# Optimization experiments

Measured on AMD Instinct MI355X. Metric: run time of the kernel, lower is better.

## Reference

```python
import jax, jax.numpy as jnp
import numpy as np

B, F, R, O = 32768, 64, 64, 64  # batch, in_features, rules, out_features


def setup_inputs() -> dict:
    key = jax.random.key(0)
    k1, k2, k3, k4, k5 = jax.random.split(key, 5)
    X = jax.random.normal(k1, (B, F), dtype=jnp.float32)
    tt = jax.random.normal(k2, (1, F, R), dtype=jnp.float32) * 0.01
    mean = jax.random.normal(k3, (1, F, R), dtype=jnp.float32)
    # std is a learned positive scale (set by _rule_initialization); keep it away from 0
    std = jax.random.uniform(k4, (1, F, R), dtype=jnp.float32, minval=0.5, maxval=1.5)
    W = jax.random.normal(k5, (O, R * (F + 1)), dtype=jnp.float32) * 0.02  # nn.Linear weight [out, in]
    return {"X": X, "tt": tt, "mean": mean, "std": std, "W": W}


def reference(X, tt, mean, std, W):
    t = jnp.tanh(tt)                                  # [1,F,R]
    z = (X[:, :, None] - mean) / std                  # [B,F,R]
    g = jnp.exp(-(z * z))                             # Gaussian membership [B,F,R]
    m = g * t + 0.5 * (1.0 - t)                       # affine blend toward 0.5
    fire = jnp.prod(m, axis=1)                        # product t-norm over features -> [B,R]
    w = fire / jnp.sum(fire, axis=1, keepdims=True)   # normalize over rules
    ones = jnp.ones((X.shape[0], 1), dtype=X.dtype)
    Xa = jnp.concatenate([X, ones], axis=1)           # [B,F+1]
    feat = (Xa[:, :, None] * w[:, None, :]).reshape(X.shape[0], -1)  # [B,(F+1)*R], row-major (f outer, r inner)
    return feat @ W.T                                 # [B,O]
```

## Files before the change

kernel.cpp:

```cpp
#include <hip/hip_runtime.h>
#include <hip/hip_bf16.h>

#define F 64
#define R 64
#define O 64
#define BLOCK_B 32

typedef short bf16x8 __attribute__((ext_vector_type(8)));
typedef float f32x4 __attribute__((ext_vector_type(4)));

static __device__ __forceinline__ short f2bf(float f) {
    unsigned u = __builtin_bit_cast(unsigned, f);
    unsigned r = (u + 0x7fffu + ((u >> 16) & 1u)) >> 16;
    return (short)r;
}

__global__ __launch_bounds__(256) void fq_prep(
        const float* __restrict__ tt, const float* __restrict__ mean,
        const float* __restrict__ std_, const float* __restrict__ W,
        float* __restrict__ prm, unsigned short* __restrict__ Wpk)
{
    const int tg = blockIdx.x * 256 + threadIdx.x;
    if (tg < 65 * 512) {
        const int f    = tg >> 9;
        const int u8   = tg & 511;
        const int lane = u8 & 63;
        const int kk   = (u8 >> 6) & 1;
        const int nt   = u8 >> 7;
        const int o    = nt * 16 + (lane & 15);
        const int rb   = ((lane >> 4) << 3) + kk * 32;
        const float* src = W + o * 4160 + f * 64 + rb;
        unsigned short v[8];
#pragma unroll
        for (int j = 0; j < 8; ++j) v[j] = (unsigned short)f2bf(src[j]);
        *(bf16x8*)(Wpk + (size_t)tg * 8) = *(bf16x8*)v;
    } else if (tg < 65 * 512 + 4096) {
        const int u = tg - 65 * 512;
        float sd = std_[u];
        float mn = mean[u];
        float th = tanhf(tt[u]);
        float s  = 1.2011224087864498f / sd;
        float4 p;
        p.x = s;
        p.y = mn * s;
        p.z = th;
        p.w = 0.5f * (1.0f - th);
        ((float4*)prm)[u] = p;
    }
}

__global__ __launch_bounds__(512, 8) void fq_main(
        const float* __restrict__ X,
        const float4* __restrict__ prm,
        const bf16x8* __restrict__ Wp,
        float* __restrict__ out)
{
    __shared__ float xt[64][BLOCK_B];
    __shared__ float fire_lds[BLOCK_B][R + 1];
    __shared__ float rinv[BLOCK_B];

    const int t    = threadIdx.x;
    const int lane = t & 63;
    const int w    = __builtin_amdgcn_readfirstlane(t >> 6);
    const int b0   = blockIdx.x * BLOCK_B;

    {
        const int row = t >> 4;
        const int f4  = (t & 15) * 4;
        float4 xv = *(const float4*)(X + (size_t)(b0 + row) * 64 + f4);
        xt[f4 + 0][row] = xv.x;
        xt[f4 + 1][row] = xv.y;
        xt[f4 + 2][row] = xv.z;
        xt[f4 + 3][row] = xv.w;
    }

    float fire[4] = {1.f, 1.f, 1.f, 1.f};
    for (int f = 0; f < F; ++f) {
        float4 p = prm[f * 64 + lane];
#pragma unroll
        for (int i = 0; i < 4; ++i) {
            float x = X[(size_t)(b0 + 4 * w + i) * 64 + f];
            float z = __builtin_fmaf(x, p.x, -p.y);
            float g = __builtin_amdgcn_exp2f(-(z * z));
            fire[i] *= __builtin_fmaf(g, p.z, p.w);
        }
    }
#pragma unroll
    for (int i = 0; i < 4; ++i)
        fire_lds[4 * w + i][lane] = fire[i];
    __syncthreads();

    if (t < BLOCK_B) {
        float s = 0.0f;
#pragma unroll 8
        for (int r = 0; r < 64; ++r) s += fire_lds[t][r];
        rinv[t] = 1.0f / s;
    }
    __syncthreads();

    const int m_in  = lane & 15;
    const int quad  = lane >> 4;
    const int mrow  = w & 1;
    const int nt    = w >> 1;
    const int myrow = 16 * mrow + m_in;
    const float rs  = rinv[myrow];

    bf16x8 wfrag[2];
#pragma unroll
    for (int kk = 0; kk < 2; ++kk)
#pragma unroll
        for (int j = 0; j < 8; ++j)
            wfrag[kk][j] = f2bf(fire_lds[myrow][quad * 8 + j + kk * 32] * rs);

    f32x4 acc = (f32x4){0.f, 0.f, 0.f, 0.f};
    const f32x4 z4 = (f32x4){0.f, 0.f, 0.f, 0.f};
    const int xoff = 16 * mrow + quad * 4;

    for (int f = 0; f < F; ++f) {
        bf16x8 bf0 = Wp[f * 512 + nt * 128 + lane];
        bf16x8 bf1 = Wp[f * 512 + nt * 128 + 64 + lane];
        f32x4 U = __builtin_amdgcn_mfma_f32_16x16x32_bf16(wfrag[0], bf0, z4, 0, 0, 0);
        U = __builtin_amdgcn_mfma_f32_16x16x32_bf16(wfrag[1], bf1, U, 0, 0, 0);
        f32x4 xv = *(const f32x4*)(&xt[f][xoff]);
#pragma unroll
        for (int reg = 0; reg < 4; ++reg)
            acc[reg] = __builtin_fmaf(xv[reg], U[reg], acc[reg]);
    }

    {
        bf16x8 bf0 = Wp[64 * 512 + nt * 128 + lane];
        bf16x8 bf1 = Wp[64 * 512 + nt * 128 + 64 + lane];
        f32x4 U = __builtin_amdgcn_mfma_f32_16x16x32_bf16(wfrag[0], bf0, z4, 0, 0, 0);
        U = __builtin_amdgcn_mfma_f32_16x16x32_bf16(wfrag[1], bf1, U, 0, 0, 0);
#pragma unroll
        for (int reg = 0; reg < 4; ++reg)
            acc[reg] += U[reg];
    }

#pragma unroll
    for (int reg = 0; reg < 4; ++reg) {
        int row = b0 + 16 * mrow + quad * 4 + reg;
        out[(size_t)row * 64 + nt * 16 + m_in] = acc[reg];
    }
}

extern "C" void kernel_launch(void* const* d_in, const int* in_sizes, int n_in,
                              void* d_out, int out_size, void* d_ws, size_t ws_size,
                              hipStream_t stream) {
    const float* X    = (const float*)d_in[0];
    const float* tt   = (const float*)d_in[1];
    const float* mean = (const float*)d_in[2];
    const float* std_ = (const float*)d_in[3];
    const float* W    = (const float*)d_in[4];
    float* out = (float*)d_out;

    float* prm = (float*)d_ws;
    unsigned short* Wpk = (unsigned short*)((char*)d_ws + 65536);

    fq_prep<<<146, 256, 0, stream>>>(tt, mean, std_, W, prm, Wpk);

    const int nblocks = 32768 / BLOCK_B;
    fq_main<<<nblocks, 512, 0, stream>>>(X, (const float4*)prm,
                                         (const bf16x8*)Wpk, out);
}
```

Baseline: 114.5 us.

## Double batch tile, read X from LDS, restructure weight packing and rule-sum reduction

The main kernel now handles 64 batch rows per 1024-thread block. The membership loop reads X from the transposed LDS tile instead of issuing scalar global loads. The row-sum over rules is done by 512 threads using vector LDS reads and shuffle reductions rather than by 32 serial threads. The prep kernel stages W through LDS for coalesced reads and repacks bf16 weights so that each n-tile's fragments are contiguous. The larger blocks may reduce occupancy and put more pressure on LDS.

```diff
diff --git a/kernel.cpp b/kernel.cpp
--- a/kernel.cpp
+++ b/kernel.cpp
@@ -4,10 +4,11 @@
 #define F 64
 #define R 64
 #define O 64
-#define BLOCK_B 32
+#define BLOCK_B 64
 
 typedef short bf16x8 __attribute__((ext_vector_type(8)));
 typedef float f32x4 __attribute__((ext_vector_type(4)));
+typedef float f32x2 __attribute__((ext_vector_type(2)));
 
 static __device__ __forceinline__ short f2bf(float f) {
     unsigned u = __builtin_bit_cast(unsigned, f);
@@ -20,43 +21,62 @@
         const float* __restrict__ std_, const float* __restrict__ W,
         float* __restrict__ prm, unsigned short* __restrict__ Wpk)
 {
-    const int tg = blockIdx.x * 256 + threadIdx.x;
-    if (tg < 65 * 512) {
-        const int f    = tg >> 9;
-        const int u8   = tg & 511;
-        const int lane = u8 & 63;
-        const int kk   = (u8 >> 6) & 1;
-        const int nt   = u8 >> 7;
-        const int o    = nt * 16 + (lane & 15);
-        const int rb   = ((lane >> 4) << 3) + kk * 32;
-        const float* src = W + o * 4160 + f * 64 + rb;
-        unsigned short v[8];
-#pragma unroll
-        for (int j = 0; j < 8; ++j) v[j] = (unsigned short)f2bf(src[j]);
-        *(bf16x8*)(Wpk + (size_t)tg * 8) = *(bf16x8*)v;
-    } else if (tg < 65 * 512 + 4096) {
-        const int u = tg - 65 * 512;
-        float sd = std_[u];
-        float mn = mean[u];
-        float th = tanhf(tt[u]);
-        float s  = 1.2011224087864498f / sd;
-        float4 p;
-        p.x = s;
-        p.y = mn * s;
-        p.z = th;
-        p.w = 0.5f * (1.0f - th);
-        ((float4*)prm)[u] = p;
-    }
-}
-
-__global__ __launch_bounds__(512, 8) void fq_main(
+    const int blk = blockIdx.x;
+    const int t   = threadIdx.x;
+    if (blk < 65) {
+        const int f = blk;
+        __shared__ __align__(16) float ws[64][68];
+#pragma unroll
+        for (int i = 0; i < 16; ++i) {
+            const int o = i * 4 + (t >> 6);
+            const int r = t & 63;
+            ws[o][r] = W[(size_t)o * 4160 + f * 64 + r];
+        }
+        __syncthreads();
+#pragma unroll
+        for (int half = 0; half < 2; ++half) {
+            const int u8   = half * 256 + t;
+            const int lane = u8 & 63;
+            const int kk   = (u8 >> 6) & 1;
+            const int nt   = u8 >> 7;
+            const int o    = nt * 16 + (lane & 15);
+            const int rb   = ((lane >> 4) << 3) + kk * 32;
+            f32x4 a = *(const f32x4*)&ws[o][rb];
+            f32x4 b = *(const f32x4*)&ws[o][rb + 4];
+            unsigned short v[8];
+            v[0] = (unsigned short)f2bf(a[0]); v[1] = (unsigned short)f2bf(a[1]);
+            v[2] = (unsigned short)f2bf(a[2]); v[3] = (unsigned short)f2bf(a[3]);
+            v[4] = (unsigned short)f2bf(b[0]); v[5] = (unsigned short)f2bf(b[1]);
+            v[6] = (unsigned short)f2bf(b[2]); v[7] = (unsigned short)f2bf(b[3]);
+            const int dst = ((nt * 65 + f) * 2 + kk) * 64 + lane;
+            *(bf16x8*)(Wpk + (size_t)dst * 8) = *(bf16x8*)v;
+        }
+    } else {
+#pragma unroll
+        for (int i = 0; i < 16; ++i) {
+            const int u = i * 256 + t;
+            float sd = std_[u];
+            float mn = mean[u];
+            float th = tanhf(tt[u]);
+            float s  = 1.2011224087864498f / sd;
+            float4 p;
+            p.x = s;
+            p.y = mn * s;
+            p.z = th;
+            p.w = 0.5f * (1.0f - th);
+            ((float4*)prm)[u] = p;
+        }
+    }
+}
+
+__global__ __launch_bounds__(1024, 8) void fq_main(
         const float* __restrict__ X,
         const float4* __restrict__ prm,
         const bf16x8* __restrict__ Wp,
         float* __restrict__ out)
 {
-    __shared__ float xt[64][BLOCK_B];
-    __shared__ float fire_lds[BLOCK_B][R + 1];
+    __shared__ __align__(16) float xt[64][68];
+    __shared__ __align__(16) float fire_lds[64][68];
     __shared__ float rinv[BLOCK_B];
 
     const int t    = threadIdx.x;
@@ -65,73 +85,99 @@
     const int b0   = blockIdx.x * BLOCK_B;
 
     {
-        const int row = t >> 4;
-        const int f4  = (t & 15) * 4;
+        const int row = t & 63;
+        const int f4  = (t >> 6) * 4;
         float4 xv = *(const float4*)(X + (size_t)(b0 + row) * 64 + f4);
         xt[f4 + 0][row] = xv.x;
         xt[f4 + 1][row] = xv.y;
         xt[f4 + 2][row] = xv.z;
         xt[f4 + 3][row] = xv.w;
     }
-
-    float fire[4] = {1.f, 1.f, 1.f, 1.f};
-    for (int f = 0; f < F; ++f) {
-        float4 p = prm[f * 64 + lane];
-#pragma unroll
-        for (int i = 0; i < 4; ++i) {
-            float x = X[(size_t)(b0 + 4 * w + i) * 64 + f];
-            float z = __builtin_fmaf(x, p.x, -p.y);
-            float g = __builtin_amdgcn_exp2f(-(z * z));
-            fire[i] *= __builtin_fmaf(g, p.z, p.w);
-        }
-    }
-#pragma unroll
-    for (int i = 0; i < 4; ++i)
-        fire_lds[4 * w + i][lane] = fire[i];
     __syncthreads();
 
-    if (t < BLOCK_B) {
-        float s = 0.0f;
-#pragma unroll 8
-        for (int r = 0; r < 64; ++r) s += fire_lds[t][r];
-        rinv[t] = 1.0f / s;
+    {
+        f32x2 fire2[2] = {(f32x2){1.f, 1.f}, (f32x2){1.f, 1.f}};
+        const int r0 = 4 * w;
+#pragma unroll 4
+        for (int f = 0; f < F; ++f) {
+            float4 p = prm[f * 64 + lane];
+            f32x2 x01 = *(const f32x2*)&xt[f][r0];
+            f32x2 x23 = *(const f32x2*)&xt[f][r0 + 2];
+            f32x2 z0, z1;
+            z0.x = __builtin_fmaf(x01.x, p.x, -p.y);
+            z0.y = __builtin_fmaf(x01.y, p.x, -p.y);
+            z1.x = __builtin_fmaf(x23.x, p.x, -p.y);
+            z1.y = __builtin_fmaf(x23.y, p.x, -p.y);
+            f32x2 nz0 = -(z0 * z0), nz1 = -(z1 * z1);
+            f32x2 g0, g1;
+            g0.x = __builtin_amdgcn_exp2f(nz0.x);
+            g0.y = __builtin_amdgcn_exp2f(nz0.y);
+            g1.x = __builtin_amdgcn_exp2f(nz1.x);
+            g1.y = __builtin_amdgcn_exp2f(nz1.y);
+            f32x2 t2 = (f32x2){p.z, p.z};
+            f32x2 c2 = (f32x2){p.w, p.w};
+            fire2[0] *= g0 * t2 + c2;
+            fire2[1] *= g1 * t2 + c2;
+        }
+        fire_lds[r0 + 0][lane] = fire2[0].x;
+        fire_lds[r0 + 1][lane] = fire2[0].y;
+        fire_lds[r0 + 2][lane] = fire2[1].x;
+        fire_lds[r0 + 3][lane] = fire2[1].y;
+    }
+    __syncthreads();
+
+    if (t < 512) {
+        const int row = t >> 3;
+        const int c8  = (t & 7) * 8;
+        f32x4 s0 = *(const f32x4*)&fire_lds[row][c8];
+        f32x4 s1 = *(const f32x4*)&fire_lds[row][c8 + 4];
+        float s = (s0[0] + s0[1]) + (s0[2] + s0[3]) +
+                  (s1[0] + s1[1]) + (s1[2] + s1[3]);
+        s += __shfl_xor(s, 1);
+        s += __shfl_xor(s, 2);
+        s += __shfl_xor(s, 4);
+        if ((t & 7) == 0) rinv[row] = 1.0f / s;
     }
     __syncthreads();
 
     const int m_in  = lane & 15;
     const int quad  = lane >> 4;
-    const int mrow  = w & 1;
-    const int nt    = w >> 1;
+    const int nt    = w >> 2;
+    const int mrow  = w & 3;
     const int myrow = 16 * mrow + m_in;
     const float rs  = rinv[myrow];
+    const int q8    = quad * 8;
 
     bf16x8 wfrag[2];
 #pragma unroll
     for (int kk = 0; kk < 2; ++kk)
 #pragma unroll
         for (int j = 0; j < 8; ++j)
-            wfrag[kk][j] = f2bf(fire_lds[myrow][quad * 8 + j + kk * 32] * rs);
+            wfrag[kk][j] = f2bf(fire_lds[myrow][q8 + j + kk * 32] * rs);
+
+    const bf16x8* wpb = Wp + (size_t)(nt * 130) * 64 + lane;
+    const int xoff = 16 * mrow + quad * 4;
 
     f32x4 acc = (f32x4){0.f, 0.f, 0.f, 0.f};
     const f32x4 z4 = (f32x4){0.f, 0.f, 0.f, 0.f};
-    const int xoff = 16 * mrow + quad * 4;
-
+
+#pragma unroll 4
     for (int f = 0; f < F; ++f) {
-        bf16x8 bf0 = Wp[f * 512 + nt * 128 + lane];
-        bf16x8 bf1 = Wp[f * 512 + nt * 128 + 64 + lane];
-        f32x4 U = __builtin_amdgcn_mfma_f32_16x16x32_bf16(wfrag[0], bf0, z4, 0, 0, 0);
-        U = __builtin_amdgcn_mfma_f32_16x16x32_bf16(wfrag[1], bf1, U, 0, 0, 0);
-        f32x4 xv = *(const f32x4*)(&xt[f][xoff]);
+        bf16x8 bb0 = wpb[(2 * f) * 64];
+        bf16x8 bb1 = wpb[(2 * f + 1) * 64];
+        f32x4 U = __builtin_amdgcn_mfma_f32_16x16x32_bf16(wfrag[0], bb0, z4, 0, 0, 0);
+        U = __builtin_amdgcn_mfma_f32_16x16x32_bf16(wfrag[1], bb1, U, 0, 0, 0);
+        f32x4 xv = *(const f32x4*)&xt[f][xoff];
 #pragma unroll
         for (int reg = 0; reg < 4; ++reg)
             acc[reg] = __builtin_fmaf(xv[reg], U[reg], acc[reg]);
     }
 
     {
-        bf16x8 bf0 = Wp[64 * 512 + nt * 128 + lane];
-        bf16x8 bf1 = Wp[64 * 512 + nt * 128 + 64 + lane];
-        f32x4 U = __builtin_amdgcn_mfma_f32_16x16x32_bf16(wfrag[0], bf0, z4, 0, 0, 0);
-        U = __builtin_amdgcn_mfma_f32_16x16x32_bf16(wfrag[1], bf1, U, 0, 0, 0);
+        bf16x8 bb0 = wpb[128 * 64];
+        bf16x8 bb1 = wpb[129 * 64];
+        f32x4 U = __builtin_amdgcn_mfma_f32_16x16x32_bf16(wfrag[0], bb0, z4, 0, 0, 0);
+        U = __builtin_amdgcn_mfma_f32_16x16x32_bf16(wfrag[1], bb1, U, 0, 0, 0);
 #pragma unroll
         for (int reg = 0; reg < 4; ++reg)
             acc[reg] += U[reg];
@@ -139,7 +185,7 @@
 
 #pragma unroll
     for (int reg = 0; reg < 4; ++reg) {
-        int row = b0 + 16 * mrow + quad * 4 + reg;
+        const int row = b0 + 16 * mrow + quad * 4 + reg;
         out[(size_t)row * 64 + nt * 16 + m_in] = acc[reg];
     }
 }
@@ -157,9 +203,9 @@
     float* prm = (float*)d_ws;
     unsigned short* Wpk = (unsigned short*)((char*)d_ws + 65536);
 
-    fq_prep<<<146, 256, 0, stream>>>(tt, mean, std_, W, prm, Wpk);
+    fq_prep<<<66, 256, 0, stream>>>(tt, mean, std_, W, prm, Wpk);
 
     const int nblocks = 32768 / BLOCK_B;
-    fq_main<<<nblocks, 512, 0, stream>>>(X, (const float4*)prm,
-                                         (const bf16x8*)Wpk, out);
-}
+    fq_main<<<nblocks, 1024, 0, stream>>>(X, (const float4*)prm,
+                                          (const bf16x8*)Wpk, out);
+}
```

After: 120.3 us. 5.0% more time.
